# Optimization experiments

Hardware: AMD Instinct MI355X
Metric: run time of the kernel (lower is better)

Reference implementation:

```python
import jax, jax.numpy as jnp
import numpy as np

TYPE_NUM = 40000
REL_NUM = 10000
N = TYPE_NUM + REL_NUM  # 50000 nodes
E = 800000              # edges (avg degree 16)
EMB, MID, OUT = 256, 256, 128


def setup_inputs() -> dict:
    key = jax.random.key(0)
    k0, k1, k2, k3 = jax.random.split(key, 4)
    # xavier-ish scales
    node_emb = jax.random.normal(k0, (N, EMB), jnp.float32) * (1.0 / np.sqrt(EMB))
    W1 = jax.random.normal(k1, (EMB, MID), jnp.float32) * (1.0 / np.sqrt(EMB))
    W2 = jax.random.normal(k2, (MID, OUT), jnp.float32) * (1.0 / np.sqrt(MID))
    b1 = jnp.zeros((MID,), jnp.float32)
    b2 = jnp.zeros((OUT,), jnp.float32)
    edge_index = jax.random.randint(k3, (2, E), 0, N, jnp.int32)
    return {"node_emb": node_emb, "W1": W1, "b1": b1, "W2": W2, "b2": b2,
            "edge_index": edge_index}


def _gcn_conv(X, W, b, src, dst):
    """torch_geometric GCNConv: x' = D^-1/2 (A+I) D^-1/2 (X W) + b."""
    n = X.shape[0]
    loop = jnp.arange(n, dtype=src.dtype)
    s = jnp.concatenate([src, loop])  # source j
    d = jnp.concatenate([dst, loop])  # target i
    deg = jax.ops.segment_sum(jnp.ones_like(d, dtype=X.dtype), d, num_segments=n)
    dis = jnp.where(deg > 0, jax.lax.rsqrt(deg), 0.0)
    h = X @ W                               # [n, out]
    norm = (dis[s] * dis[d])[:, None]       # [E+n, 1]
    msg = h[s] * norm                       # gather messages
    return jax.ops.segment_sum(msg, d, num_segments=n) + b


def reference(node_emb, W1, b1, W2, b2, edge_index):
    src, dst = edge_index[0], edge_index[1]
    # torch nn.GELU default is exact (erf) gelu
    X = jax.nn.gelu(_gcn_conv(node_emb, W1, b1, src, dst), approximate=False)
    X = jax.nn.gelu(_gcn_conv(X, W2, b2, src, dst), approximate=False)
    return X[:TYPE_NUM], X[TYPE_NUM:]
```

## Files before the change

kernel.cpp:

```cpp
#include <hip/hip_runtime.h>
#include <math.h>

#define EMB 256
#define MID 256
#define OUTF 128
#define KDIM 256
#define LDK 40
#define SLOT 64

using frag_ab = __attribute__((ext_vector_type(8))) short;
using frag_cd = __attribute__((ext_vector_type(4))) float;
typedef float f32x2 __attribute__((ext_vector_type(2)));
typedef float f32x4 __attribute__((ext_vector_type(4)));
typedef unsigned int u32x2 __attribute__((ext_vector_type(2)));
typedef unsigned int u32x4 __attribute__((ext_vector_type(4)));

__device__ __forceinline__ float gelu_exact(float x) {
    return 0.5f * x * (1.0f + erff(x * 0.70710678118654752f));
}

__device__ __forceinline__ unsigned short f2bf(float f) {
    union { float f; unsigned int i; } v;
    v.f = f;
    unsigned int r = v.i + 0x7fff + ((v.i >> 16) & 1);
    return (unsigned short)(r >> 16);
}

__device__ __forceinline__ f32x2 bfpair(unsigned int u) {
    union { unsigned int i; float f; } a, b;
    a.i = u << 16;
    b.i = u & 0xffff0000u;
    f32x2 r;
    r.x = a.f; r.y = b.f;
    return r;
}


__global__ __launch_bounds__(256) void init_kernel(
    const float* __restrict__ W1, const float* __restrict__ W2,
    unsigned short* __restrict__ W1t, unsigned short* __restrict__ W2t,
    int* __restrict__ cnt, unsigned short* __restrict__ h1,
    unsigned short* __restrict__ h2, int n, int zb) {
    int b = blockIdx.x;
    int tid = threadIdx.x;
    if (b < zb) {
        int i = b * 256 + tid;
        if (i < n) cnt[i] = 0;
        return;
    }
    b -= zb;
    if (b < 256) {
        int id = b * 256 + tid;
        int k = id >> 8, nn = id & 255;
        W1t[(size_t)nn * EMB + k] = f2bf(W1[(size_t)k * MID + nn]);
        return;
    }
    b -= 256;
    if (b < 128) {
        int id = b * 256 + tid;
        int k = id >> 7, nn = id & 127;
        W2t[(size_t)nn * MID + k] = f2bf(W2[(size_t)k * OUTF + nn]);
        return;
    }
    size_t Np1 = (size_t)n + 1;
    int s = tid >> 5, c = tid & 31;
    h1[((size_t)s * Np1 + n) * 32 + c] = 0;
    if (tid < 128) h2[((size_t)s * Np1 + n) * 32 + c] = 0;
}


__global__ void rank_scatter(const int* __restrict__ src, const int* __restrict__ dst,
                             int* __restrict__ cnt, unsigned short* __restrict__ slots,
                             int E) {
    int e = blockIdx.x * blockDim.x + threadIdx.x;
    if (e < E) {
        int d = dst[e];
        int r = atomicAdd(&cnt[d], 1);
        if (r < SLOT) slots[(size_t)d * SLOT + r] = (unsigned short)src[e];
    }
}


template <bool A_FP32, int NT>
__global__ __launch_bounds__(256, 2) void mfma_gemm(const void* __restrict__ Av,
                                                    const unsigned short* __restrict__ Wt,
                                                    const int* __restrict__ cnt,
                                                    unsigned short* __restrict__ C,
                                                    int M, int Cs) {
    __shared__ __align__(16) unsigned short As[128 * LDK];
    __shared__ __align__(16) unsigned short Bs[NT * 128 * LDK];

    const int tid = threadIdx.x;
    const int m0 = blockIdx.x * 128;
    const int wave = tid >> 6, lane = tid & 63;
    const int wrow = (wave >> 1) * 64, wcol = (wave & 1) * 64;
    const int q = lane >> 4, r = lane & 15;

    frag_cd acc[NT][4][4] = {};

    const int qb = tid & 3;
    const int nb = tid >> 2;

    for (int ks = 0; ks < KDIM; ks += 32) {
        if (A_FP32) {
            const float* A = (const float*)Av;
            int qa = tid & 7;
            int ra = tid >> 3;
#pragma unroll
            for (int rr = 0; rr < 4; ++rr) {
                int row = ra + rr * 32;
                int grow = m0 + row;
                if (grow >= M) grow = M - 1;
                float4 v = *(const float4*)(A + (size_t)grow * KDIM + ks + qa * 4);
                ushort4 w;
                w.x = f2bf(v.x); w.y = f2bf(v.y); w.z = f2bf(v.z); w.w = f2bf(v.w);
                *(ushort4*)&As[row * LDK + qa * 4] = w;
            }
        } else {
            const unsigned short* A = (const unsigned short*)Av;
#pragma unroll
            for (int rr = 0; rr < 2; ++rr) {
                int row = nb + rr * 64;
                int grow = m0 + row;
                if (grow >= M) grow = M - 1;
                uint4 v = *(const uint4*)(A + ((size_t)(ks >> 5) * M + grow) * 32 + qb * 8);
                *(uint4*)&As[row * LDK + qb * 8] = v;
            }
        }
#pragma unroll
        for (int rr = 0; rr < 2 * NT; ++rr) {
            int n = nb + rr * 64;
            uint4 v = *(const uint4*)(Wt + (size_t)n * KDIM + ks + qb * 8);
            *(uint4*)&Bs[n * LDK + qb * 8] = v;
        }
        __syncthreads();

        frag_ab af[4];
#pragma unroll
        for (int i = 0; i < 4; ++i)
            af[i] = *(const frag_ab*)&As[(wrow + i * 16 + r) * LDK + q * 8];
#pragma unroll
        for (int nt = 0; nt < NT; ++nt) {
            frag_ab bfr[4];
#pragma unroll
            for (int j = 0; j < 4; ++j)
                bfr[j] = *(const frag_ab*)&Bs[(nt * 128 + wcol + j * 16 + r) * LDK + q * 8];
#pragma unroll
            for (int i = 0; i < 4; ++i)
#pragma unroll
                for (int j = 0; j < 4; ++j)
                    acc[nt][i][j] = __builtin_amdgcn_mfma_f32_16x16x32_bf16(
                        af[i], bfr[j], acc[nt][i][j], 0, 0, 0);
        }
        __syncthreads();
    }

#pragma unroll
    for (int i = 0; i < 4; ++i)
#pragma unroll
        for (int g = 0; g < 4; ++g) {
            int row = m0 + wrow + i * 16 + q * 4 + g;
            if (row < M) {
                float sc = rsqrtf((float)(cnt[row] + 1));
#pragma unroll
                for (int nt = 0; nt < NT; ++nt)
#pragma unroll
                    for (int j = 0; j < 4; ++j) {
                        int col = nt * 128 + wcol + j * 16 + r;
                        C[((size_t)(col >> 5) * Cs + row) * 32 + (col & 31)] =
                            f2bf(acc[nt][i][j][g] * sc);
                    }
            }
        }
}


template <int NS, bool OUT_BF>
__global__ __launch_bounds__(256, 4) void agg_slice(
    const unsigned short* __restrict__ H,
    const int* __restrict__ cnt,
    const unsigned short* __restrict__ slots,
    const float* __restrict__ bias,
    void* __restrict__ out,
    int n) {
    constexpr int XPS = 8 / NS;
    const int bid = blockIdx.x;
    const int xg = bid & 7;
    const int s = xg / XPS;
    const int w = (bid >> 3) * XPS + (xg % XPS);
    const int W = (int)(gridDim.x >> 3) * XPS;
    const int wave = threadIdx.x >> 6, lane = threadIdx.x & 63;
    const int g = lane >> 3, r = lane & 7;
    const size_t Np1 = (size_t)n + 1;
    const unsigned short* Hs = H + (size_t)s * Np1 * 32;
    const float4 bv = *(const float4*)(bias + s * 32 + r * 4);
    const int r4 = r * 4;

    for (int nd0 = (w * 4 + wave) * 8; nd0 < n; nd0 += W * 32) {
        int ndg = nd0 + g;
        bool valid = ndg < n;
        int ndc = valid ? ndg : n - 1;
        int deg = cnt[ndc];
        float di = rsqrtf((float)(deg + 1));
        int m = valid ? (deg < SLOT ? deg : SLOT) : 0;
        int mm = m;
        mm = max(mm, __shfl_xor(mm, 8));
        mm = max(mm, __shfl_xor(mm, 16));
        mm = max(mm, __shfl_xor(mm, 32));

        uint2 sv = *(const uint2*)(Hs + (size_t)ndc * 32 + r4);
        f32x2 a01 = bfpair(sv.x), a23 = bfpair(sv.y);

        const unsigned short* sl = slots + (size_t)ndc * SLOT;
        u32x4 sq = {};
        if (r * 8 < mm) sq = __builtin_nontemporal_load((const u32x4*)(sl + r * 8));

        if (mm > 0) {
            uint2 A[8], B[8];
            auto load8 = [&](uint2* buf, int t) {
                int srcl = (lane & 56) | (t >> 3);
                unsigned w0 = (unsigned)__shfl((int)sq.x, srcl);
                unsigned w1 = (unsigned)__shfl((int)sq.y, srcl);
                unsigned w2 = (unsigned)__shfl((int)sq.z, srcl);
                unsigned w3 = (unsigned)__shfl((int)sq.w, srcl);
                int j0 = (t + 0 < m) ? (int)(w0 & 0xffffu) : n;
                int j1 = (t + 1 < m) ? (int)(w0 >> 16) : n;
                int j2 = (t + 2 < m) ? (int)(w1 & 0xffffu) : n;
                int j3 = (t + 3 < m) ? (int)(w1 >> 16) : n;
                int j4 = (t + 4 < m) ? (int)(w2 & 0xffffu) : n;
                int j5 = (t + 5 < m) ? (int)(w2 >> 16) : n;
                int j6 = (t + 6 < m) ? (int)(w3 & 0xffffu) : n;
                int j7 = (t + 7 < m) ? (int)(w3 >> 16) : n;
                buf[0] = *(const uint2*)(Hs + (size_t)j0 * 32 + r4);
                buf[1] = *(const uint2*)(Hs + (size_t)j1 * 32 + r4);
                buf[2] = *(const uint2*)(Hs + (size_t)j2 * 32 + r4);
                buf[3] = *(const uint2*)(Hs + (size_t)j3 * 32 + r4);
                buf[4] = *(const uint2*)(Hs + (size_t)j4 * 32 + r4);
                buf[5] = *(const uint2*)(Hs + (size_t)j5 * 32 + r4);
                buf[6] = *(const uint2*)(Hs + (size_t)j6 * 32 + r4);
                buf[7] = *(const uint2*)(Hs + (size_t)j7 * 32 + r4);
            };
            auto acc8 = [&](const uint2* buf) {
#pragma unroll
                for (int u = 0; u < 8; ++u) {
                    a01 += bfpair(buf[u].x);
                    a23 += bfpair(buf[u].y);
                }
            };

            load8(A, 0);
            int t = 8;
            for (;;) {
                if (t >= mm) { acc8(A); break; }
                load8(B, t); acc8(A); t += 8;
                if (t >= mm) { acc8(B); break; }
                load8(A, t); acc8(B); t += 8;
            }
        }

        float r0 = gelu_exact(di * a01.x + bv.x);
        float r1 = gelu_exact(di * a01.y + bv.y);
        float r2 = gelu_exact(di * a23.x + bv.z);
        float r3 = gelu_exact(di * a23.y + bv.w);

        if (valid) {
            if (OUT_BF) {
                u32x2 pk;
                pk.x = (unsigned int)f2bf(r0) | ((unsigned int)f2bf(r1) << 16);
                pk.y = (unsigned int)f2bf(r2) | ((unsigned int)f2bf(r3) << 16);
                unsigned short* ob = (unsigned short*)out + ((size_t)s * n + ndg) * 32 + r4;
                __builtin_nontemporal_store(pk, (u32x2*)ob);
            } else {
                f32x4 rv;
                rv.x = r0; rv.y = r1; rv.z = r2; rv.w = r3;
                float* ob = (float*)out + (size_t)ndg * (NS * 32) + s * 32 + r4;
                __builtin_nontemporal_store(rv, (f32x4*)ob);
            }
        }
    }
}


extern "C" void kernel_launch(void* const* d_in, const int* in_sizes, int n_in,
                              void* d_out, int out_size, void* d_ws, size_t ws_size,
                              hipStream_t stream) {
    const float* node_emb = (const float*)d_in[0];
    const float* W1 = (const float*)d_in[1];
    const float* b1 = (const float*)d_in[2];
    const float* W2 = (const float*)d_in[3];
    const float* b2 = (const float*)d_in[4];
    const int* edge_index = (const int*)d_in[5];

    const int N = in_sizes[0] / EMB;
    const int E = in_sizes[5] / 2;
    const int* src = edge_index;
    const int* dst = edge_index + E;

    char* ws = (char*)d_ws;
    size_t off = 0;
    auto alloc = [&](size_t bytes) -> void* {
        off = (off + 255) & ~(size_t)255;
        void* p = ws + off;
        off += bytes;
        return p;
    };

    const int nb = (N + 255) / 256;

    int* cnt = (int*)alloc((size_t)N * 4);
    unsigned short* slots = (unsigned short*)alloc((size_t)N * SLOT * 2);
    unsigned short* W1t = (unsigned short*)alloc((size_t)EMB * MID * 2);
    unsigned short* W2t = (unsigned short*)alloc((size_t)MID * OUTF * 2);
    unsigned short* h1 = (unsigned short*)alloc((size_t)(N + 1) * MID * 2);
    unsigned short* h2 = (unsigned short*)alloc((size_t)(N + 1) * OUTF * 2);
    unsigned short* X1 = (unsigned short*)alloc((size_t)N * MID * 2);

    init_kernel<<<nb + 256 + 128 + 1, 256, 0, stream>>>(
        W1, W2, W1t, W2t, cnt, h1, h2, N, nb);
    rank_scatter<<<(E + 255) / 256, 256, 0, stream>>>(src, dst, cnt, slots, E);
    mfma_gemm<true, 2><<<(N + 127) / 128, 256, 0, stream>>>(node_emb, W1t, cnt, h1, N, N + 1);
    agg_slice<8, true><<<2048, 256, 0, stream>>>(h1, cnt, slots, b1, X1, N);
    mfma_gemm<false, 1><<<(N + 127) / 128, 256, 0, stream>>>(X1, W2t, cnt, h2, N, N + 1);
    agg_slice<4, false><<<2048, 256, 0, stream>>>(h2, cnt, slots, b2, d_out, N);
}
```

Before: 285.7 us.

## Sort nodes by degree for aggregation and widen per-lane gather to 16B

Adds a histogram, scan and scatter pass that builds a degree-sorted permutation of nodes. The aggregation kernels walk nodes in that order, so the 16 nodes sharing a wave have similar neighbour counts and the loop runs to a shared maximum with less divergence. Each lane now loads 8 bf16 values (16 bytes) per neighbour instead of 4, with 4 lanes per node, and issues 4 gathers per step instead of 8. It costs three extra small kernel launches and scatters output writes in permuted order, which loses locality.

```diff
diff --git a/kernel.cpp b/kernel.cpp
--- a/kernel.cpp
+++ b/kernel.cpp
@@ -7,6 +7,7 @@
 #define KDIM 256
 #define LDK 40
 #define SLOT 64
+#define NBIN 64
 
 using frag_ab = __attribute__((ext_vector_type(8))) short;
 using frag_cd = __attribute__((ext_vector_type(4))) float;
@@ -40,7 +41,7 @@
     const float* __restrict__ W1, const float* __restrict__ W2,
     unsigned short* __restrict__ W1t, unsigned short* __restrict__ W2t,
     int* __restrict__ cnt, unsigned short* __restrict__ h1,
-    unsigned short* __restrict__ h2, int n, int zb) {
+    unsigned short* __restrict__ h2, int* __restrict__ ghist, int n, int zb) {
     int b = blockIdx.x;
     int tid = threadIdx.x;
     if (b < zb) {
@@ -66,6 +67,7 @@
     int s = tid >> 5, c = tid & 31;
     h1[((size_t)s * Np1 + n) * 32 + c] = 0;
     if (tid < 128) h2[((size_t)s * Np1 + n) * 32 + c] = 0;
+    if (tid < NBIN) ghist[tid] = 0;
 }
 
 
@@ -81,6 +83,54 @@
 }
 
 
+__global__ __launch_bounds__(256) void deg_hist(const int* __restrict__ cnt,
+                                                int* __restrict__ ghist, int n) {
+    __shared__ int lh[NBIN];
+    int tid = threadIdx.x;
+    if (tid < NBIN) lh[tid] = 0;
+    __syncthreads();
+    int i = blockIdx.x * 256 + tid;
+    if (i < n) {
+        int d = cnt[i];
+        d = d < NBIN - 1 ? d : NBIN - 1;
+        atomicAdd(&lh[d], 1);
+    }
+    __syncthreads();
+    if (tid < NBIN && lh[tid]) atomicAdd(&ghist[tid], lh[tid]);
+}
+
+__global__ void deg_scan(const int* __restrict__ ghist, int* __restrict__ goff) {
+    int v = ghist[threadIdx.x];
+    int x = v;
+#pragma unroll
+    for (int d = 1; d < NBIN; d <<= 1) {
+        int t = __shfl_up(x, d);
+        if ((int)threadIdx.x >= d) x += t;
+    }
+    goff[threadIdx.x] = x - v;
+}
+
+__global__ __launch_bounds__(256) void deg_scatter(const int* __restrict__ cnt,
+                                                   int* __restrict__ goff,
+                                                   int* __restrict__ perm, int n) {
+    __shared__ int lh[NBIN], lbase[NBIN];
+    int tid = threadIdx.x;
+    if (tid < NBIN) lh[tid] = 0;
+    __syncthreads();
+    int i = blockIdx.x * 256 + tid;
+    int d = 0, rl = 0;
+    if (i < n) {
+        d = cnt[i];
+        d = d < NBIN - 1 ? d : NBIN - 1;
+        rl = atomicAdd(&lh[d], 1);
+    }
+    __syncthreads();
+    if (tid < NBIN) lbase[tid] = lh[tid] ? atomicAdd(&goff[tid], lh[tid]) : 0;
+    __syncthreads();
+    if (i < n) perm[lbase[d] + rl] = i;
+}
+
+
 template <bool A_FP32, int NT>
 __global__ __launch_bounds__(256, 2) void mfma_gemm(const void* __restrict__ Av,
                                                     const unsigned short* __restrict__ Wt,
@@ -180,6 +230,7 @@
     const unsigned short* __restrict__ H,
     const int* __restrict__ cnt,
     const unsigned short* __restrict__ slots,
+    const int* __restrict__ perm,
     const float* __restrict__ bias,
     void* __restrict__ out,
     int n) {
@@ -190,91 +241,98 @@
     const int w = (bid >> 3) * XPS + (xg % XPS);
     const int W = (int)(gridDim.x >> 3) * XPS;
     const int wave = threadIdx.x >> 6, lane = threadIdx.x & 63;
-    const int g = lane >> 3, r = lane & 7;
+    const int g = lane >> 2, r = lane & 3;
     const size_t Np1 = (size_t)n + 1;
     const unsigned short* Hs = H + (size_t)s * Np1 * 32;
-    const float4 bv = *(const float4*)(bias + s * 32 + r * 4);
-    const int r4 = r * 4;
-
-    for (int nd0 = (w * 4 + wave) * 8; nd0 < n; nd0 += W * 32) {
-        int ndg = nd0 + g;
-        bool valid = ndg < n;
-        int ndc = valid ? ndg : n - 1;
-        int deg = cnt[ndc];
+    const int r8 = r * 8;
+    const f32x4 bv0 = *(const f32x4*)(bias + s * 32 + r8);
+    const f32x4 bv1 = *(const f32x4*)(bias + s * 32 + r8 + 4);
+
+    for (int nd0 = (w * 4 + wave) * 16; nd0 < n; nd0 += W * 64) {
+        int idx = nd0 + g;
+        bool valid = idx < n;
+        int ndg = perm[valid ? idx : n - 1];
+        int deg = cnt[ndg];
         float di = rsqrtf((float)(deg + 1));
         int m = valid ? (deg < SLOT ? deg : SLOT) : 0;
         int mm = m;
+        mm = max(mm, __shfl_xor(mm, 4));
         mm = max(mm, __shfl_xor(mm, 8));
         mm = max(mm, __shfl_xor(mm, 16));
         mm = max(mm, __shfl_xor(mm, 32));
 
-        uint2 sv = *(const uint2*)(Hs + (size_t)ndc * 32 + r4);
-        f32x2 a01 = bfpair(sv.x), a23 = bfpair(sv.y);
-
-        const unsigned short* sl = slots + (size_t)ndc * SLOT;
-        u32x4 sq = {};
-        if (r * 8 < mm) sq = __builtin_nontemporal_load((const u32x4*)(sl + r * 8));
+        u32x4 sv = *(const u32x4*)(Hs + (size_t)ndg * 32 + r8);
+        f32x2 a0 = bfpair(sv.x), a1 = bfpair(sv.y), a2 = bfpair(sv.z), a3 = bfpair(sv.w);
+
+        const unsigned short* sl = slots + (size_t)ndg * SLOT;
+        u32x4 sq0 = {}, sq1 = {};
+        if (r8 < m) sq0 = __builtin_nontemporal_load((const u32x4*)(sl + r8));
+        if (32 + r8 < m) sq1 = __builtin_nontemporal_load((const u32x4*)(sl + 32 + r8));
 
         if (mm > 0) {
-            uint2 A[8], B[8];
-            auto load8 = [&](uint2* buf, int t) {
-                int srcl = (lane & 56) | (t >> 3);
-                unsigned w0 = (unsigned)__shfl((int)sq.x, srcl);
-                unsigned w1 = (unsigned)__shfl((int)sq.y, srcl);
-                unsigned w2 = (unsigned)__shfl((int)sq.z, srcl);
-                unsigned w3 = (unsigned)__shfl((int)sq.w, srcl);
+            u32x4 A[4], B[4];
+            auto load4 = [&](u32x4* buf, int t) {
+                int srcl = (lane & 60) | ((t >> 3) & 3);
+                u32x4 sq = (t < 32) ? sq0 : sq1;
+                unsigned hw0, hw1;
+                if (t & 4) { hw0 = sq.z; hw1 = sq.w; } else { hw0 = sq.x; hw1 = sq.y; }
+                unsigned w0 = (unsigned)__shfl((int)hw0, srcl);
+                unsigned w1 = (unsigned)__shfl((int)hw1, srcl);
                 int j0 = (t + 0 < m) ? (int)(w0 & 0xffffu) : n;
                 int j1 = (t + 1 < m) ? (int)(w0 >> 16) : n;
                 int j2 = (t + 2 < m) ? (int)(w1 & 0xffffu) : n;
                 int j3 = (t + 3 < m) ? (int)(w1 >> 16) : n;
-                int j4 = (t + 4 < m) ? (int)(w2 & 0xffffu) : n;
-                int j5 = (t + 5 < m) ? (int)(w2 >> 16) : n;
-                int j6 = (t + 6 < m) ? (int)(w3 & 0xffffu) : n;
-                int j7 = (t + 7 < m) ? (int)(w3 >> 16) : n;
-                buf[0] = *(const uint2*)(Hs + (size_t)j0 * 32 + r4);
-                buf[1] = *(const uint2*)(Hs + (size_t)j1 * 32 + r4);
-                buf[2] = *(const uint2*)(Hs + (size_t)j2 * 32 + r4);
-                buf[3] = *(const uint2*)(Hs + (size_t)j3 * 32 + r4);
-                buf[4] = *(const uint2*)(Hs + (size_t)j4 * 32 + r4);
-                buf[5] = *(const uint2*)(Hs + (size_t)j5 * 32 + r4);
-                buf[6] = *(const uint2*)(Hs + (size_t)j6 * 32 + r4);
-                buf[7] = *(const uint2*)(Hs + (size_t)j7 * 32 + r4);
+                buf[0] = *(const u32x4*)(Hs + (size_t)j0 * 32 + r8);
+                buf[1] = *(const u32x4*)(Hs + (size_t)j1 * 32 + r8);
+                buf[2] = *(const u32x4*)(Hs + (size_t)j2 * 32 + r8);
+                buf[3] = *(const u32x4*)(Hs + (size_t)j3 * 32 + r8);
             };
-            auto acc8 = [&](const uint2* buf) {
-#pragma unroll
-                for (int u = 0; u < 8; ++u) {
-                    a01 += bfpair(buf[u].x);
-                    a23 += bfpair(buf[u].y);
+            auto acc4 = [&](const u32x4* buf) {
+#pragma unroll
+                for (int u = 0; u < 4; ++u) {
+                    a0 += bfpair(buf[u].x);
+                    a1 += bfpair(buf[u].y);
+                    a2 += bfpair(buf[u].z);
+                    a3 += bfpair(buf[u].w);
                 }
             };
 
-            load8(A, 0);
-            int t = 8;
+            load4(A, 0);
+            int t = 4;
             for (;;) {
-                if (t >= mm) { acc8(A); break; }
-                load8(B, t); acc8(A); t += 8;
-                if (t >= mm) { acc8(B); break; }
-                load8(A, t); acc8(B); t += 8;
-            }
-        }
-
-        float r0 = gelu_exact(di * a01.x + bv.x);
-        float r1 = gelu_exact(di * a01.y + bv.y);
-        float r2 = gelu_exact(di * a23.x + bv.z);
-        float r3 = gelu_exact(di * a23.y + bv.w);
+                if (t >= mm) { acc4(A); break; }
+                load4(B, t); acc4(A); t += 4;
+                if (t >= mm) { acc4(B); break; }
+                load4(A, t); acc4(B); t += 4;
+            }
+        }
+
+        float res[8];
+        res[0] = gelu_exact(di * a0.x + bv0.x);
+        res[1] = gelu_exact(di * a0.y + bv0.y);
+        res[2] = gelu_exact(di * a1.x + bv0.z);
+        res[3] = gelu_exact(di * a1.y + bv0.w);
+        res[4] = gelu_exact(di * a2.x + bv1.x);
+        res[5] = gelu_exact(di * a2.y + bv1.y);
+        res[6] = gelu_exact(di * a3.x + bv1.z);
+        res[7] = gelu_exact(di * a3.y + bv1.w);
 
         if (valid) {
             if (OUT_BF) {
-                u32x2 pk;
-                pk.x = (unsigned int)f2bf(r0) | ((unsigned int)f2bf(r1) << 16);
-                pk.y = (unsigned int)f2bf(r2) | ((unsigned int)f2bf(r3) << 16);
-                unsigned short* ob = (unsigned short*)out + ((size_t)s * n + ndg) * 32 + r4;
-                __builtin_nontemporal_store(pk, (u32x2*)ob);
+                u32x4 pk;
+                pk.x = (unsigned int)f2bf(res[0]) | ((unsigned int)f2bf(res[1]) << 16);
+                pk.y = (unsigned int)f2bf(res[2]) | ((unsigned int)f2bf(res[3]) << 16);
+                pk.z = (unsigned int)f2bf(res[4]) | ((unsigned int)f2bf(res[5]) << 16);
+                pk.w = (unsigned int)f2bf(res[6]) | ((unsigned int)f2bf(res[7]) << 16);
+                unsigned short* ob = (unsigned short*)out + ((size_t)s * n + ndg) * 32 + r8;
+                __builtin_nontemporal_store(pk, (u32x4*)ob);
             } else {
-                f32x4 rv;
-                rv.x = r0; rv.y = r1; rv.z = r2; rv.w = r3;
-                float* ob = (float*)out + (size_t)ndg * (NS * 32) + s * 32 + r4;
-                __builtin_nontemporal_store(rv, (f32x4*)ob);
+                f32x4 rv0, rv1;
+                rv0.x = res[0]; rv0.y = res[1]; rv0.z = res[2]; rv0.w = res[3];
+                rv1.x = res[4]; rv1.y = res[5]; rv1.z = res[6]; rv1.w = res[7];
+                float* ob = (float*)out + (size_t)ndg * (NS * 32) + s * 32 + r8;
+                __builtin_nontemporal_store(rv0, (f32x4*)ob);
+                __builtin_nontemporal_store(rv1, (f32x4*)(ob + 4));
             }
         }
     }
@@ -314,12 +372,18 @@
     unsigned short* h1 = (unsigned short*)alloc((size_t)(N + 1) * MID * 2);
     unsigned short* h2 = (unsigned short*)alloc((size_t)(N + 1) * OUTF * 2);
     unsigned short* X1 = (unsigned short*)alloc((size_t)N * MID * 2);
+    int* ghist = (int*)alloc(NBIN * 4);
+    int* goff = (int*)alloc(NBIN * 4);
+    int* perm = (int*)alloc((size_t)N * 4);
 
     init_kernel<<<nb + 256 + 128 + 1, 256, 0, stream>>>(
-        W1, W2, W1t, W2t, cnt, h1, h2, N, nb);
+        W1, W2, W1t, W2t, cnt, h1, h2, ghist, N, nb);
     rank_scatter<<<(E + 255) / 256, 256, 0, stream>>>(src, dst, cnt, slots, E);
+    deg_hist<<<nb, 256, 0, stream>>>(cnt, ghist, N);
+    deg_scan<<<1, NBIN, 0, stream>>>(ghist, goff);
+    deg_scatter<<<nb, 256, 0, stream>>>(cnt, goff, perm, N);
     mfma_gemm<true, 2><<<(N + 127) / 128, 256, 0, stream>>>(node_emb, W1t, cnt, h1, N, N + 1);
-    agg_slice<8, true><<<2048, 256, 0, stream>>>(h1, cnt, slots, b1, X1, N);
+    agg_slice<8, true><<<2048, 256, 0, stream>>>(h1, cnt, slots, perm, b1, X1, N);
     mfma_gemm<false, 1><<<(N + 127) / 128, 256, 0, stream>>>(X1, W2t, cnt, h2, N, N + 1);
-    agg_slice<4, false><<<2048, 256, 0, stream>>>(h2, cnt, slots, b2, d_out, N);
-}
+    agg_slice<4, false><<<2048, 256, 0, stream>>>(h2, cnt, slots, perm, b2, d_out, N);
+}
```

Result: faster. 272.4 us (-4.6%).
